# Performance work log

Hardware: AMD Instinct MI355X
Metric: run time of the kernel (lower is better)

## Reference

```python
import jax, jax.numpy as jnp
import numpy as np

B, T, D = 2, 1024, 2048
H, KV, Dh = 16, 4, 128
REP = H // KV
LAMBDA_INIT = 0.8 - 0.6 * float(np.exp(-0.3 * 0))  # depth=0 -> 0.2
ROPE_THETA = 10000.0


def rope_cos_sin(pos, dh):
    # standard rotary embedding tables, half-split (rotate_half) convention
    inv_freq = 1.0 / (ROPE_THETA ** (jnp.arange(0, dh, 2, dtype=jnp.float32) / dh))
    freqs = pos.astype(jnp.float32)[:, None] * inv_freq[None, :]  # (T, Dh/2)
    return jnp.cos(freqs), jnp.sin(freqs)


def apply_rope(x, cos, sin):
    # x: (B, H, T, Dh); cos/sin: (T, Dh/2)
    x1, x2 = jnp.split(x, 2, axis=-1)
    c = cos[None, None, :, :]
    s = sin[None, None, :, :]
    return jnp.concatenate([x1 * c - x2 * s, x1 * s + x2 * c], axis=-1)


def setup_inputs() -> dict:
    key = jax.random.key(0)
    ks = jax.random.split(key, 5)
    std = 0.02
    return {
        "x": jax.random.normal(ks[0], (B, T, D), dtype=jnp.float32),
        "wq": jax.random.normal(ks[1], (D, 2 * H * Dh), dtype=jnp.float32) * std,
        "wk": jax.random.normal(ks[2], (D, 2 * KV * Dh), dtype=jnp.float32) * std,
        "wv": jax.random.normal(ks[3], (D, 2 * KV * Dh), dtype=jnp.float32) * std,
        "wo": jax.random.normal(ks[4], (2 * H * Dh, D), dtype=jnp.float32) * std,
    }


def reference(x, wq, wk, wv, wo):
    # projections (no bias)
    q = (x @ wq).reshape(B, T, H, 2 * Dh).transpose(0, 2, 1, 3)    # (B,H,T,2Dh)
    k = (x @ wk).reshape(B, T, KV, 2 * Dh).transpose(0, 2, 1, 3)   # (B,KV,T,2Dh)
    v = (x @ wv).reshape(B, T, KV, 2 * Dh).transpose(0, 2, 1, 3)   # (B,KV,T,2Dh)

    q1, q2 = jnp.split(q, 2, axis=-1)
    k1, k2 = jnp.split(k, 2, axis=-1)

    pos = jnp.arange(T)
    cos, sin = rope_cos_sin(pos, Dh)
    q1 = apply_rope(q1, cos, sin)
    q2 = apply_rope(q2, cos, sin)
    k1 = apply_rope(k1, cos, sin)
    k2 = apply_rope(k2, cos, sin)

    # GQA: repeat kv heads contiguously (matches expand+reshape)
    k1f = jnp.repeat(k1, REP, axis=1)
    k2f = jnp.repeat(k2, REP, axis=1)
    vf = jnp.repeat(v, REP, axis=1)  # (B,H,T,2Dh)

    scale = 1.0 / jnp.sqrt(jnp.float32(Dh))
    scores1 = jnp.einsum("bhtd,bhsd->bhts", q1, k1f) * scale
    scores2 = jnp.einsum("bhtd,bhsd->bhts", q2, k2f) * scale

    causal = jnp.triu(jnp.ones((T, T), dtype=bool), k=1)  # True above diagonal
    neg_inf = jnp.float32(-jnp.inf)
    scores1 = jnp.where(causal[None, None], neg_inf, scores1)
    scores2 = jnp.where(causal[None, None], neg_inf, scores2)

    attn1 = jax.nn.softmax(scores1, axis=-1)
    attn2 = jax.nn.softmax(scores2, axis=-1)
    attn_diff = attn1 - LAMBDA_INIT * attn2

    out = jnp.einsum("bhts,bhsd->bhtd", attn_diff, vf)  # (B,H,T,2Dh)
    out = out.transpose(0, 2, 1, 3).reshape(B, T, 2 * H * Dh)
    return out @ wo  # (B,T,D)
```

## Files before the change

kernel.cpp:

```cpp
#include <hip/hip_runtime.h>
#include <hip/hip_bf16.h>
#include <stdint.h>

typedef __bf16 bf16_t;
typedef __attribute__((ext_vector_type(8))) __bf16 bf16x8;
typedef __attribute__((ext_vector_type(4))) __bf16 bf16x4;
typedef __attribute__((ext_vector_type(4))) float f32x4;

#define AS1 __attribute__((address_space(1)))
#define AS3 __attribute__((address_space(3)))

__device__ inline void gload_lds16(const void* g, void* l) {
    __builtin_amdgcn_global_load_lds((AS1 void*)(uintptr_t)g, (AS3 void*)l, 16, 0, 0);
}

__device__ inline f32x4 mfma_bf16_16x16x32(bf16x8 a, bf16x8 b, f32x4 c) {
    return __builtin_amdgcn_mfma_f32_16x16x32_bf16(a, b, c, 0, 0, 0);
}


__global__ __launch_bounds__(256) void cast_x_kernel(const float* __restrict__ x,
                                                     bf16_t* __restrict__ xb, int n) {
    int i = (blockIdx.x * 256 + threadIdx.x) * 4;
    if (i >= n) return;
    float4 v = *reinterpret_cast<const float4*>(x + i);
    bf16x4 o;
    o[0] = (bf16_t)v.x; o[1] = (bf16_t)v.y; o[2] = (bf16_t)v.z; o[3] = (bf16_t)v.w;
    *reinterpret_cast<bf16x4*>(xb + i) = o;
}

__global__ __launch_bounds__(256) void transpose_cast_w(const float* __restrict__ s0,
                                                        const float* __restrict__ s1,
                                                        const float* __restrict__ s2,
                                                        int n1, int n2,
                                                        int ld0, int ld1, int ld2,
                                                        int K, int N, bf16_t* __restrict__ dst) {
    __shared__ float tile[32][33];
    const int kt = blockIdx.x * 32, nt = blockIdx.y * 32;
    const int tx = threadIdx.x & 31, ty = threadIdx.x >> 5;
    #pragma unroll
    for (int j = 0; j < 4; j++) {
        int k = kt + ty + j * 8;
        int n = nt + tx;
        float v;
        if (n < n1)      v = s0[(size_t)k * ld0 + n];
        else if (n < n2) v = s1[(size_t)k * ld1 + (n - n1)];
        else             v = s2[(size_t)k * ld2 + (n - n2)];
        tile[ty + j * 8][tx] = v;
    }
    __syncthreads();
    #pragma unroll
    for (int j = 0; j < 4; j++) {
        int n = nt + ty + j * 8;
        int k = kt + tx;
        dst[(size_t)n * K + k] = (bf16_t)tile[tx][ty + j * 8];
    }
}

__global__ __launch_bounds__(256) void rope_qk(bf16_t* __restrict__ qkv) {
    int tid = blockIdx.x * 256 + threadIdx.x;
    int i = tid & 63;
    int u = (tid >> 6) % 40;
    int row = tid / 2560;
    int base;
    if (u < 32) base = (u >> 1) * 256 + (u & 1) * 128;
    else { int uu = u - 32; base = 4096 + (uu >> 1) * 256 + (uu & 1) * 128; }
    bf16_t* p = qkv + (size_t)row * 6144 + base;
    float x1 = (float)p[i];
    float x2 = (float)p[i + 64];
    int t = row & 1023;
    float invf = exp2f(-0.20762050593045893f * (float)i);
    float a = (float)t * invf;
    float c = cosf(a), s = sinf(a);
    p[i]      = (bf16_t)(x1 * c - x2 * s);
    p[i + 64] = (bf16_t)(x1 * s + x2 * c);
}

__global__ __launch_bounds__(256) void pack_vt(const bf16_t* __restrict__ qkv,
                                               bf16_t* __restrict__ vt) {
    __shared__ bf16_t tile[32][33];
    const int st = blockIdx.x * 32, dt = blockIdx.y * 32, bkv = blockIdx.z;
    const int b = bkv >> 2, kv = bkv & 3;
    const int tx = threadIdx.x & 31, ty = threadIdx.x >> 5;
    #pragma unroll
    for (int j = 0; j < 4; j++) {
        int s = st + ty + j * 8;
        tile[ty + j * 8][tx] = qkv[(size_t)(b * 1024 + s) * 6144 + 5120 + kv * 256 + dt + tx];
    }
    __syncthreads();
    #pragma unroll
    for (int j = 0; j < 4; j++) {
        int d = dt + ty + j * 8;
        vt[(size_t)(bkv * 256 + d) * 1024 + st + tx] = tile[tx][ty + j * 8];
    }
}

template <int BN, int OUT_BF16>
__global__ __launch_bounds__(256, 3) void gemm_bt(const bf16_t* __restrict__ A,
                                                  const bf16_t* __restrict__ Bt,
                                                  void* __restrict__ Cv,
                                                  int M, int N, int K) {
    constexpr int ASZ = 128 * 32;
    constexpr int BSZ = BN * 32;
    constexpr int MI = (BN == 128) ? 4 : 2;
    __shared__ bf16_t As[2 * ASZ];
    __shared__ bf16_t Bs[2 * BSZ];
    const int tid = threadIdx.x;
    const int w = tid >> 6, l = tid & 63;
    const int lq = l & 15, g = l >> 4;
    const int wrow = (BN == 128) ? ((w >> 1) * 64) : (w * 32);
    const int wcol = (BN == 128) ? ((w & 1) * 64) : 0;
    const size_t m0 = (size_t)blockIdx.x * 128;
    const size_t n0 = (size_t)blockIdx.y * BN;
    f32x4 acc[MI][4];
    #pragma unroll
    for (int i = 0; i < MI; i++)
        #pragma unroll
        for (int j = 0; j < 4; j++) { acc[i][j][0] = 0.f; acc[i][j][1] = 0.f; acc[i][j][2] = 0.f; acc[i][j][3] = 0.f; }
    const int rowi = l >> 2;
    const int ko = (l & 3) * 8;
    const bf16_t* Ab = A + (m0 + rowi) * K + ko;
    const bf16_t* Bb = Bt + (n0 + rowi) * K + ko;
    const int nt = K / 32;

    auto stage = [&](int buf, int t) {
        const int k0 = t * 32;
        #pragma unroll
        for (int j = 0; j < 2; j++) {
            const int c = j * 4 + w;
            gload_lds16(Ab + (size_t)(c * 16) * K + k0, As + buf * ASZ + c * 512);
        }
        if constexpr (BN == 128) {
            #pragma unroll
            for (int j = 0; j < 2; j++) {
                const int c = j * 4 + w;
                gload_lds16(Bb + (size_t)(c * 16) * K + k0, Bs + buf * BSZ + c * 512);
            }
        } else {
            gload_lds16(Bb + (size_t)(w * 16) * K + k0, Bs + buf * BSZ + w * 512);
        }
    };

    stage(0, 0);
    __syncthreads();
    int cur = 0;
    for (int t = 0; t < nt; t++) {
        if (t + 1 < nt) stage(cur ^ 1, t + 1);
        bf16x8 af[MI], bfv[4];
        #pragma unroll
        for (int mi = 0; mi < MI; mi++)
            af[mi] = *reinterpret_cast<const bf16x8*>(&As[cur * ASZ + (wrow + mi * 16 + lq) * 32 + g * 8]);
        #pragma unroll
        for (int ni = 0; ni < 4; ni++)
            bfv[ni] = *reinterpret_cast<const bf16x8*>(&Bs[cur * BSZ + (wcol + ni * 16 + lq) * 32 + g * 8]);
        #pragma unroll
        for (int mi = 0; mi < MI; mi++)
            #pragma unroll
            for (int ni = 0; ni < 4; ni++)
                acc[mi][ni] = mfma_bf16_16x16x32(af[mi], bfv[ni], acc[mi][ni]);
        __syncthreads();
        cur ^= 1;
    }
    #pragma unroll
    for (int mi = 0; mi < MI; mi++)
        #pragma unroll
        for (int ni = 0; ni < 4; ni++)
            #pragma unroll
            for (int r = 0; r < 4; r++) {
                size_t row = m0 + wrow + mi * 16 + 4 * g + r;
                size_t col = n0 + wcol + ni * 16 + lq;
                float v = acc[mi][ni][r];
                if (OUT_BF16) ((bf16_t*)Cv)[row * N + col] = (bf16_t)v;
                else          ((float*)Cv)[row * N + col] = v;
            }
}

__global__ __launch_bounds__(256, 3) void attn_fused(const bf16_t* __restrict__ qkv,
                                                     const bf16_t* __restrict__ vt,
                                                     bf16_t* __restrict__ ao) {
    const int bh = blockIdx.x;
    const int qt = 31 - (int)blockIdx.y;
    const int b = bh >> 4, h = bh & 15, kv = h >> 2;
    const int tid = threadIdx.x;
    const int w = tid >> 6, l = tid & 63;
    const int rg = w >> 1, wh = w & 1;
    const int lq = l & 15, g = l >> 4;
    const int q0 = qt * 32;
    const float scale = 0.08838834764831845f;

    __shared__ char smem[36864];
    bf16_t* Ks  = (bf16_t*)smem;
    bf16_t* Vs  = (bf16_t*)(smem + 16384);
    bf16_t* Ps  = (bf16_t*)(smem + 32768) + w * 512;
    bf16_t* O2s = (bf16_t*)smem;

    bf16x8 qf[4];
    {
        const bf16_t* qp = qkv + (size_t)(b * 1024 + q0 + rg * 16 + lq) * 6144 + h * 256 + wh * 128 + g * 8;
        #pragma unroll
        for (int c = 0; c < 4; c++) qf[c] = *reinterpret_cast<const bf16x8*>(qp + c * 32);
    }
    const int t = q0 + rg * 16 + lq;

    const int kr_off = l >> 5;
    const int kc16   = l & 31;
    const int vd_off = l >> 2;
    const int vc16   = l & 3;

    const bf16_t* kgbase = qkv + (size_t)(b * 1024) * 6144 + 4096 + kv * 256;
    const bf16_t* vgbase = vt + (size_t)((b * 4 + kv) * 256) * 1024;

    float m = -1e30f, lsum = 0.f;
    f32x4 oacc[16];
    #pragma unroll
    for (int dt = 0; dt < 16; dt++) { oacc[dt][0] = 0.f; oacc[dt][1] = 0.f; oacc[dt][2] = 0.f; oacc[dt][3] = 0.f; }

    const int nr = qt + 1;
    for (int rnd = 0; rnd < nr; ++rnd) {
        const int s0 = rnd * 32;
        #pragma unroll
        for (int j = 0; j < 4; j++) {
            int r = 8 * w + 2 * j + kr_off;
            int d = (kc16 ^ (r & 7)) * 8;
            gload_lds16(kgbase + (size_t)(s0 + r) * 6144 + d, Ks + (8 * w + 2 * j) * 256);
        }
        #pragma unroll
        for (int j = 0; j < 4; j++) {
            int d = 64 * w + 16 * j + vd_off;
            int sc = (vc16 ^ ((d >> 1) & 3)) * 8;
            gload_lds16(vgbase + (size_t)d * 1024 + s0 + sc, Vs + (64 * w + 16 * j) * 32);
        }
        __syncthreads();

        f32x4 stA, stB;
        stA[0] = stA[1] = stA[2] = stA[3] = 0.f;
        stB[0] = stB[1] = stB[2] = stB[3] = 0.f;
        #pragma unroll
        for (int c = 0; c < 4; c++) {
            const int c16 = wh * 16 + c * 4 + g;
            const int rA = lq, rB = 16 + lq;
            bf16x8 kfa = *reinterpret_cast<const bf16x8*>(Ks + rA * 256 + ((c16 ^ (rA & 7)) * 8));
            bf16x8 kfb = *reinterpret_cast<const bf16x8*>(Ks + rB * 256 + ((c16 ^ (rB & 7)) * 8));
            stA = mfma_bf16_16x16x32(kfa, qf[c], stA);
            stB = mfma_bf16_16x16x32(kfb, qf[c], stB);
        }
        const bool lastr = (rnd == nr - 1);
        float pA[4], pB[4];
        float tmax = -1e30f;
        #pragma unroll
        for (int r = 0; r < 4; r++) {
            float a  = stA[r] * scale;
            float bv = stB[r] * scale;
            if (lastr) {
                if (s0 + 4 * g + r > t)      a  = -1e30f;
                if (s0 + 16 + 4 * g + r > t) bv = -1e30f;
            }
            pA[r] = a; pB[r] = bv;
            tmax = fmaxf(tmax, fmaxf(a, bv));
        }
        tmax = fmaxf(tmax, __shfl_xor(tmax, 16));
        tmax = fmaxf(tmax, __shfl_xor(tmax, 32));
        const float mnew = fmaxf(m, tmax);
        const float alpha = __expf(m - mnew);
        float ps = 0.f;
        #pragma unroll
        for (int r = 0; r < 4; r++) {
            pA[r] = __expf(pA[r] - mnew);
            pB[r] = __expf(pB[r] - mnew);
            ps += pA[r] + pB[r];
        }
        ps += __shfl_xor(ps, 16);
        ps += __shfl_xor(ps, 32);
        lsum = lsum * alpha + ps;
        m = mnew;
        float al[4];
        #pragma unroll
        for (int r = 0; r < 4; r++) al[r] = __shfl(alpha, 4 * g + r);
        #pragma unroll
        for (int dt = 0; dt < 16; dt++) {
            oacc[dt][0] *= al[0]; oacc[dt][1] *= al[1]; oacc[dt][2] *= al[2]; oacc[dt][3] *= al[3];
        }
        bf16x4 wa, wb;
        #pragma unroll
        for (int r = 0; r < 4; r++) { wa[r] = (bf16_t)pA[r]; wb[r] = (bf16_t)pB[r]; }
        *reinterpret_cast<bf16x4*>(&Ps[lq * 32 + 4 * g]) = wa;
        *reinterpret_cast<bf16x4*>(&Ps[lq * 32 + 16 + 4 * g]) = wb;
        bf16x8 pf = *reinterpret_cast<const bf16x8*>(&Ps[lq * 32 + 8 * g]);
        #pragma unroll
        for (int dt = 0; dt < 16; dt++) {
            const int d = dt * 16 + lq;
            bf16x8 vf = *reinterpret_cast<const bf16x8*>(Vs + d * 32 + ((g ^ ((d >> 1) & 3)) * 8));
            oacc[dt] = mfma_bf16_16x16x32(pf, vf, oacc[dt]);
        }
        __syncthreads();
    }

    float li[4];
    #pragma unroll
    for (int r = 0; r < 4; r++) li[r] = 1.0f / __shfl(lsum, 4 * g + r);

    if (wh == 1) {
        #pragma unroll
        for (int dt = 0; dt < 16; dt++)
            #pragma unroll
            for (int r = 0; r < 4; r++)
                O2s[(rg * 16 + 4 * g + r) * 256 + dt * 16 + lq] = (bf16_t)(oacc[dt][r] * li[r]);
    }
    __syncthreads();
    if (wh == 0) {
        #pragma unroll
        for (int dt = 0; dt < 16; dt++)
            #pragma unroll
            for (int r = 0; r < 4; r++) {
                const int qloc = rg * 16 + 4 * g + r;
                float o2 = (float)O2s[qloc * 256 + dt * 16 + lq];
                ao[(size_t)(b * 1024 + q0 + qloc) * 4096 + h * 256 + dt * 16 + lq] =
                    (bf16_t)(oacc[dt][r] * li[r] - 0.2f * o2);
            }
    }
}


extern "C" void kernel_launch(void* const* d_in, const int* in_sizes, int n_in,
                              void* d_out, int out_size, void* d_ws, size_t ws_size,
                              hipStream_t stream) {
    (void)in_sizes; (void)n_in; (void)out_size;
    const float* x  = (const float*)d_in[0];
    const float* wq = (const float*)d_in[1];
    const float* wk = (const float*)d_in[2];
    const float* wv = (const float*)d_in[3];
    const float* wo = (const float*)d_in[4];

    char* ws = (char*)d_ws;
    size_t off = 0;
    auto alloc = [&](size_t bytes) {
        void* p = ws + off;
        off += (bytes + 255) & ~(size_t)255;
        return p;
    };
    bf16_t* xb   = (bf16_t*)alloc(4194304ull * 2);
    bf16_t* wbt  = (bf16_t*)alloc(6144ull * 2048 * 2);
    bf16_t* wot  = (bf16_t*)alloc(2048ull * 4096 * 2);
    bf16_t* qkvb = (bf16_t*)alloc(2048ull * 6144 * 2);
    bf16_t* vtb  = (bf16_t*)alloc(8ull * 256 * 1024 * 2);
    bf16_t* ao   = (bf16_t*)alloc(2048ull * 4096 * 2);
    if (off > ws_size) return;

    cast_x_kernel<<<4096, 256, 0, stream>>>(x, xb, 4194304);
    transpose_cast_w<<<dim3(64, 192), 256, 0, stream>>>(wq, wk, wv, 4096, 5120,
                                                        4096, 1024, 1024, 2048, 6144, wbt);
    transpose_cast_w<<<dim3(128, 64), 256, 0, stream>>>(wo, wo, wo, 1 << 28, 1 << 28,
                                                        2048, 2048, 2048, 4096, 2048, wot);
    gemm_bt<128, 1><<<dim3(16, 48), 256, 0, stream>>>(xb, wbt, qkvb, 2048, 6144, 2048);
    rope_qk<<<20480, 256, 0, stream>>>(qkvb);
    pack_vt<<<dim3(32, 8, 8), 256, 0, stream>>>(qkvb, vtb);
    attn_fused<<<dim3(32, 32), 256, 0, stream>>>(qkvb, vtb, ao);
    gemm_bt<64, 0><<<dim3(16, 32), 256, 0, stream>>>(ao, wot, (float*)d_out, 2048, 2048, 4096);
}
```

Measured before the change: 241.8 us.

## Halve attention block to two waves each processing two query row tiles

The attention kernel now runs 128 threads per block, and each wave handles both 16-row query tiles instead of one. Each K fragment and V fragment read from LDS is reused for two MFMAs, and each wave issues twice as many global-to-LDS loads. It also adds a lazy softmax rescale that only updates the running max and rescales the accumulators when the new block max exceeds the old one by more than 8. The P staging buffer is padded to a 40-element row stride to reduce LDS bank conflicts. In exchange the doubled accumulator state raises register pressure, and with fewer waves per block there may be less latency hiding.

```diff
diff --git a/kernel.cpp b/kernel.cpp
--- a/kernel.cpp
+++ b/kernel.cpp
@@ -175,32 +175,31 @@
             }
 }
 
-__global__ __launch_bounds__(256, 3) void attn_fused(const bf16_t* __restrict__ qkv,
+__global__ __launch_bounds__(128, 2) void attn_fused(const bf16_t* __restrict__ qkv,
                                                      const bf16_t* __restrict__ vt,
                                                      bf16_t* __restrict__ ao) {
     const int bh = blockIdx.x;
     const int qt = 31 - (int)blockIdx.y;
     const int b = bh >> 4, h = bh & 15, kv = h >> 2;
     const int tid = threadIdx.x;
-    const int w = tid >> 6, l = tid & 63;
-    const int rg = w >> 1, wh = w & 1;
+    const int wh = tid >> 6, l = tid & 63;
     const int lq = l & 15, g = l >> 4;
     const int q0 = qt * 32;
     const float scale = 0.08838834764831845f;
 
-    __shared__ char smem[36864];
+    __shared__ char smem[16384 + 16384 + 2 * 2560];
     bf16_t* Ks  = (bf16_t*)smem;
     bf16_t* Vs  = (bf16_t*)(smem + 16384);
-    bf16_t* Ps  = (bf16_t*)(smem + 32768) + w * 512;
+    bf16_t* Psb = (bf16_t*)(smem + 32768 + wh * 2560);
     bf16_t* O2s = (bf16_t*)smem;
 
-    bf16x8 qf[4];
-    {
-        const bf16_t* qp = qkv + (size_t)(b * 1024 + q0 + rg * 16 + lq) * 6144 + h * 256 + wh * 128 + g * 8;
-        #pragma unroll
-        for (int c = 0; c < 4; c++) qf[c] = *reinterpret_cast<const bf16x8*>(qp + c * 32);
-    }
-    const int t = q0 + rg * 16 + lq;
+    bf16x8 qf[2][4];
+    #pragma unroll
+    for (int ct = 0; ct < 2; ct++) {
+        const bf16_t* qp = qkv + (size_t)(b * 1024 + q0 + ct * 16 + lq) * 6144 + h * 256 + wh * 128 + g * 8;
+        #pragma unroll
+        for (int c = 0; c < 4; c++) qf[ct][c] = *reinterpret_cast<const bf16x8*>(qp + c * 32);
+    }
 
     const int kr_off = l >> 5;
     const int kc16   = l & 31;
@@ -210,113 +209,142 @@
     const bf16_t* kgbase = qkv + (size_t)(b * 1024) * 6144 + 4096 + kv * 256;
     const bf16_t* vgbase = vt + (size_t)((b * 4 + kv) * 256) * 1024;
 
-    float m = -1e30f, lsum = 0.f;
-    f32x4 oacc[16];
-    #pragma unroll
-    for (int dt = 0; dt < 16; dt++) { oacc[dt][0] = 0.f; oacc[dt][1] = 0.f; oacc[dt][2] = 0.f; oacc[dt][3] = 0.f; }
+    float m0v = -1e30f, m1v = -1e30f, ls0 = 0.f, ls1 = 0.f;
+    f32x4 oacc[2][16];
+    #pragma unroll
+    for (int ct = 0; ct < 2; ct++)
+        #pragma unroll
+        for (int dt = 0; dt < 16; dt++) { oacc[ct][dt][0] = 0.f; oacc[ct][dt][1] = 0.f; oacc[ct][dt][2] = 0.f; oacc[ct][dt][3] = 0.f; }
 
     const int nr = qt + 1;
     for (int rnd = 0; rnd < nr; ++rnd) {
         const int s0 = rnd * 32;
         #pragma unroll
-        for (int j = 0; j < 4; j++) {
-            int r = 8 * w + 2 * j + kr_off;
+        for (int j = 0; j < 8; j++) {
+            int r = 16 * wh + 2 * j + kr_off;
             int d = (kc16 ^ (r & 7)) * 8;
-            gload_lds16(kgbase + (size_t)(s0 + r) * 6144 + d, Ks + (8 * w + 2 * j) * 256);
-        }
-        #pragma unroll
-        for (int j = 0; j < 4; j++) {
-            int d = 64 * w + 16 * j + vd_off;
+            gload_lds16(kgbase + (size_t)(s0 + r) * 6144 + d, Ks + (16 * wh + 2 * j) * 256);
+        }
+        #pragma unroll
+        for (int j = 0; j < 8; j++) {
+            int d = 128 * wh + 16 * j + vd_off;
             int sc = (vc16 ^ ((d >> 1) & 3)) * 8;
-            gload_lds16(vgbase + (size_t)d * 1024 + s0 + sc, Vs + (64 * w + 16 * j) * 32);
+            gload_lds16(vgbase + (size_t)d * 1024 + s0 + sc, Vs + (128 * wh + 16 * j) * 32);
         }
         __syncthreads();
 
-        f32x4 stA, stB;
-        stA[0] = stA[1] = stA[2] = stA[3] = 0.f;
-        stB[0] = stB[1] = stB[2] = stB[3] = 0.f;
+        f32x4 st[2][2];
+        #pragma unroll
+        for (int i = 0; i < 2; i++)
+            #pragma unroll
+            for (int j = 0; j < 2; j++) { st[i][j][0] = 0.f; st[i][j][1] = 0.f; st[i][j][2] = 0.f; st[i][j][3] = 0.f; }
         #pragma unroll
         for (int c = 0; c < 4; c++) {
             const int c16 = wh * 16 + c * 4 + g;
-            const int rA = lq, rB = 16 + lq;
-            bf16x8 kfa = *reinterpret_cast<const bf16x8*>(Ks + rA * 256 + ((c16 ^ (rA & 7)) * 8));
-            bf16x8 kfb = *reinterpret_cast<const bf16x8*>(Ks + rB * 256 + ((c16 ^ (rB & 7)) * 8));
-            stA = mfma_bf16_16x16x32(kfa, qf[c], stA);
-            stB = mfma_bf16_16x16x32(kfb, qf[c], stB);
+            bf16x8 kfa = *reinterpret_cast<const bf16x8*>(Ks + lq * 256 + ((c16 ^ (lq & 7)) * 8));
+            bf16x8 kfb = *reinterpret_cast<const bf16x8*>(Ks + (16 + lq) * 256 + ((c16 ^ (lq & 7)) * 8));
+            #pragma unroll
+            for (int ct = 0; ct < 2; ct++) {
+                st[0][ct] = mfma_bf16_16x16x32(kfa, qf[ct][c], st[0][ct]);
+                st[1][ct] = mfma_bf16_16x16x32(kfb, qf[ct][c], st[1][ct]);
+            }
         }
         const bool lastr = (rnd == nr - 1);
-        float pA[4], pB[4];
-        float tmax = -1e30f;
-        #pragma unroll
-        for (int r = 0; r < 4; r++) {
-            float a  = stA[r] * scale;
-            float bv = stB[r] * scale;
-            if (lastr) {
-                if (s0 + 4 * g + r > t)      a  = -1e30f;
-                if (s0 + 16 + 4 * g + r > t) bv = -1e30f;
-            }
-            pA[r] = a; pB[r] = bv;
-            tmax = fmaxf(tmax, fmaxf(a, bv));
-        }
-        tmax = fmaxf(tmax, __shfl_xor(tmax, 16));
-        tmax = fmaxf(tmax, __shfl_xor(tmax, 32));
-        const float mnew = fmaxf(m, tmax);
-        const float alpha = __expf(m - mnew);
-        float ps = 0.f;
-        #pragma unroll
-        for (int r = 0; r < 4; r++) {
-            pA[r] = __expf(pA[r] - mnew);
-            pB[r] = __expf(pB[r] - mnew);
-            ps += pA[r] + pB[r];
-        }
-        ps += __shfl_xor(ps, 16);
-        ps += __shfl_xor(ps, 32);
-        lsum = lsum * alpha + ps;
-        m = mnew;
-        float al[4];
-        #pragma unroll
-        for (int r = 0; r < 4; r++) al[r] = __shfl(alpha, 4 * g + r);
-        #pragma unroll
-        for (int dt = 0; dt < 16; dt++) {
-            oacc[dt][0] *= al[0]; oacc[dt][1] *= al[1]; oacc[dt][2] *= al[2]; oacc[dt][3] *= al[3];
-        }
-        bf16x4 wa, wb;
-        #pragma unroll
-        for (int r = 0; r < 4; r++) { wa[r] = (bf16_t)pA[r]; wb[r] = (bf16_t)pB[r]; }
-        *reinterpret_cast<bf16x4*>(&Ps[lq * 32 + 4 * g]) = wa;
-        *reinterpret_cast<bf16x4*>(&Ps[lq * 32 + 16 + 4 * g]) = wb;
-        bf16x8 pf = *reinterpret_cast<const bf16x8*>(&Ps[lq * 32 + 8 * g]);
+        float p[2][2][4];
+        float pm0 = -1e30f, pm1 = -1e30f;
+        #pragma unroll
+        for (int half = 0; half < 2; half++)
+            #pragma unroll
+            for (int r = 0; r < 4; r++) {
+                const int sidx = s0 + half * 16 + 4 * g + r;
+                float v0 = st[half][0][r] * scale;
+                float v1 = st[half][1][r] * scale;
+                if (lastr) {
+                    if (sidx > q0 + lq)      v0 = -1e30f;
+                    if (sidx > q0 + 16 + lq) v1 = -1e30f;
+                }
+                p[half][0][r] = v0; p[half][1][r] = v1;
+                pm0 = fmaxf(pm0, v0); pm1 = fmaxf(pm1, v1);
+            }
+        pm0 = fmaxf(pm0, __shfl_xor(pm0, 16)); pm0 = fmaxf(pm0, __shfl_xor(pm0, 32));
+        pm1 = fmaxf(pm1, __shfl_xor(pm1, 16)); pm1 = fmaxf(pm1, __shfl_xor(pm1, 32));
+        const bool need = (pm0 > m0v + 8.f) || (pm1 > m1v + 8.f);
+        if (__any(need)) {
+            float mn0 = fmaxf(m0v, pm0), mn1 = fmaxf(m1v, pm1);
+            float a0 = __expf(m0v - mn0), a1 = __expf(m1v - mn1);
+            m0v = mn0; m1v = mn1;
+            ls0 *= a0; ls1 *= a1;
+            float al0[4], al1[4];
+            #pragma unroll
+            for (int r = 0; r < 4; r++) { al0[r] = __shfl(a0, 4 * g + r); al1[r] = __shfl(a1, 4 * g + r); }
+            #pragma unroll
+            for (int dt = 0; dt < 16; dt++)
+                #pragma unroll
+                for (int r = 0; r < 4; r++) { oacc[0][dt][r] *= al0[r]; oacc[1][dt][r] *= al1[r]; }
+        }
+        float ps0 = 0.f, ps1 = 0.f;
+        #pragma unroll
+        for (int half = 0; half < 2; half++)
+            #pragma unroll
+            for (int r = 0; r < 4; r++) {
+                p[half][0][r] = __expf(p[half][0][r] - m0v); ps0 += p[half][0][r];
+                p[half][1][r] = __expf(p[half][1][r] - m1v); ps1 += p[half][1][r];
+            }
+        ps0 += __shfl_xor(ps0, 16); ps0 += __shfl_xor(ps0, 32); ls0 += ps0;
+        ps1 += __shfl_xor(ps1, 16); ps1 += __shfl_xor(ps1, 32); ls1 += ps1;
+        #pragma unroll
+        for (int ct = 0; ct < 2; ct++)
+            #pragma unroll
+            for (int half = 0; half < 2; half++) {
+                bf16x4 wv;
+                #pragma unroll
+                for (int r = 0; r < 4; r++) wv[r] = (bf16_t)p[half][ct][r];
+                *reinterpret_cast<bf16x4*>(Psb + (ct * 16 + lq) * 40 + half * 16 + 4 * g) = wv;
+            }
+        bf16x8 pf[2];
+        pf[0] = *reinterpret_cast<const bf16x8*>(Psb + lq * 40 + g * 8);
+        pf[1] = *reinterpret_cast<const bf16x8*>(Psb + (16 + lq) * 40 + g * 8);
         #pragma unroll
         for (int dt = 0; dt < 16; dt++) {
             const int d = dt * 16 + lq;
             bf16x8 vf = *reinterpret_cast<const bf16x8*>(Vs + d * 32 + ((g ^ ((d >> 1) & 3)) * 8));
-            oacc[dt] = mfma_bf16_16x16x32(pf, vf, oacc[dt]);
+            oacc[0][dt] = mfma_bf16_16x16x32(pf[0], vf, oacc[0][dt]);
+            oacc[1][dt] = mfma_bf16_16x16x32(pf[1], vf, oacc[1][dt]);
         }
         __syncthreads();
     }
 
-    float li[4];
-    #pragma unroll
-    for (int r = 0; r < 4; r++) li[r] = 1.0f / __shfl(lsum, 4 * g + r);
-
+    float li0[4], li1[4];
+    #pragma unroll
+    for (int r = 0; r < 4; r++) {
+        li0[r] = 1.0f / __shfl(ls0, 4 * g + r);
+        li1[r] = 1.0f / __shfl(ls1, 4 * g + r);
+    }
     if (wh == 1) {
         #pragma unroll
-        for (int dt = 0; dt < 16; dt++)
-            #pragma unroll
-            for (int r = 0; r < 4; r++)
-                O2s[(rg * 16 + 4 * g + r) * 256 + dt * 16 + lq] = (bf16_t)(oacc[dt][r] * li[r]);
+        for (int ct = 0; ct < 2; ct++)
+            #pragma unroll
+            for (int dt = 0; dt < 16; dt++)
+                #pragma unroll
+                for (int r = 0; r < 4; r++) {
+                    const float liv = ct ? li1[r] : li0[r];
+                    O2s[(ct * 16 + 4 * g + r) * 256 + dt * 16 + lq] = (bf16_t)(oacc[ct][dt][r] * liv);
+                }
     }
     __syncthreads();
     if (wh == 0) {
         #pragma unroll
-        for (int dt = 0; dt < 16; dt++)
-            #pragma unroll
-            for (int r = 0; r < 4; r++) {
-                const int qloc = rg * 16 + 4 * g + r;
-                float o2 = (float)O2s[qloc * 256 + dt * 16 + lq];
-                ao[(size_t)(b * 1024 + q0 + qloc) * 4096 + h * 256 + dt * 16 + lq] =
-                    (bf16_t)(oacc[dt][r] * li[r] - 0.2f * o2);
-            }
+        for (int ct = 0; ct < 2; ct++)
+            #pragma unroll
+            for (int dt = 0; dt < 16; dt++)
+                #pragma unroll
+                for (int r = 0; r < 4; r++) {
+                    const int qloc = ct * 16 + 4 * g + r;
+                    const float liv = ct ? li1[r] : li0[r];
+                    float o2 = (float)O2s[qloc * 256 + dt * 16 + lq];
+                    ao[(size_t)(b * 1024 + q0 + qloc) * 4096 + h * 256 + dt * 16 + lq] =
+                        (bf16_t)(oacc[ct][dt][r] * liv - 0.2f * o2);
+                }
     }
 }
 
@@ -354,6 +382,6 @@
     gemm_bt<128, 1><<<dim3(16, 48), 256, 0, stream>>>(xb, wbt, qkvb, 2048, 6144, 2048);
     rope_qk<<<20480, 256, 0, stream>>>(qkvb);
     pack_vt<<<dim3(32, 8, 8), 256, 0, stream>>>(qkvb, vtb);
-    attn_fused<<<dim3(32, 32), 256, 0, stream>>>(qkvb, vtb, ao);
+    attn_fused<<<dim3(32, 32), 128, 0, stream>>>(qkvb, vtb, ao);
     gemm_bt<64, 0><<<dim3(16, 32), 256, 0, stream>>>(ao, wot, (float*)d_out, 2048, 2048, 4096);
 }
```

New measurement: 256.5 us. 6.1% more time.
